# Kernel tuning notes

Measured on AMD Instinct MI355X. Metric: run time of the kernel, lower is better.

## Reference

```python
import jax, jax.numpy as jnp
import numpy as np

N_QUBITS = 4 + 4  # 8
N_LAYERS = 4
DIM = 2 ** N_QUBITS


def _apply_1q(state, U, wire):
    # state: (B, 2,...,2) complex; U: (2,2) complex; contract qubit `wire`
    s = jnp.moveaxis(state, wire + 1, -1)
    s = s @ U.T  # out[..., i] = sum_j U[i, j] * s[..., j]
    return jnp.moveaxis(s, -1, wire + 1)


def _apply_cnot(state, c, t):
    s = jnp.moveaxis(state, (c + 1, t + 1), (-2, -1))  # (..., 2c, 2t)
    s = jnp.concatenate([s[..., 0:1, :], s[..., 1:2, ::-1]], axis=-2)
    return jnp.moveaxis(s, (-2, -1), (c + 1, t + 1))


def _quantum_layer(q_in, qw):
    """Batched statevector sim: RY(pi*x) encoding + StronglyEntanglingLayers + <Z_i>."""
    B = q_in.shape[0]
    # RY(a)|0> = cos(a/2)|0> + sin(a/2)|1>, a = pi * x  -> product state
    half = q_in * (jnp.pi / 2)
    qvecs = jnp.stack([jnp.cos(half), jnp.sin(half)], axis=-1).astype(jnp.complex64)  # (B, n, 2)
    state = qvecs[:, 0]
    for i in range(1, N_QUBITS):
        state = (state[:, :, None] * qvecs[:, i][:, None, :]).reshape(B, -1)
    state = state.reshape((B,) + (2,) * N_QUBITS)
    # Rot(phi, theta, omega) = RZ(omega) RY(theta) RZ(phi)
    phi, theta, omega = qw[..., 0], qw[..., 1], qw[..., 2]
    c, s = jnp.cos(theta / 2), jnp.sin(theta / 2)
    m00 = jnp.exp(-0.5j * (phi + omega)) * c
    m01 = -jnp.exp(0.5j * (phi - omega)) * s
    m10 = jnp.exp(-0.5j * (phi - omega)) * s
    m11 = jnp.exp(0.5j * (phi + omega)) * c
    rot = jnp.stack([jnp.stack([m00, m01], -1), jnp.stack([m10, m11], -1)], -2)  # (L, n, 2, 2)
    rot = rot.astype(jnp.complex64)
    for l in range(N_LAYERS):
        for w in range(N_QUBITS):
            state = _apply_1q(state, rot[l, w], w)
        r = (l % (N_QUBITS - 1)) + 1  # PennyLane default ranges
        for w in range(N_QUBITS):
            state = _apply_cnot(state, w, (w + r) % N_QUBITS)
    amps = state.reshape(B, DIM)
    probs = jnp.real(amps * jnp.conj(amps))  # (B, 2^n) float32
    # <Z_i> = sum_b probs_b * (+1 if bit_i(b)==0 else -1); wire 0 = most significant axis
    idx = np.arange(DIM)
    bits = (idx[None, :] >> (N_QUBITS - 1 - np.arange(N_QUBITS))[:, None]) & 1  # (n, 2^n)
    zvals = jnp.asarray(1.0 - 2.0 * bits, dtype=jnp.float32)
    return probs @ zvals.T  # (B, n)


def _forward(x, w_pre1, b_pre1, w_pre2, b_pre2, w_pre3, b_pre3, qw,
             w_post1, b_post1, w_post2, b_post2, w_post3, b_post3):
    # eval mode: dropout is identity
    h = jax.nn.relu(x @ w_pre1 + b_pre1)
    h = jax.nn.relu(h @ w_pre2 + b_pre2)
    q_in = jnp.tanh(h @ w_pre3 + b_pre3)          # (B, n_qubits)
    z = _quantum_layer(q_in, qw)                   # (B, n_qubits)
    h = jax.nn.relu(z @ w_post1 + b_post1)
    h = jax.nn.relu(h @ w_post2 + b_post2)
    return h @ w_post3 + b_post3                   # (B, num_classes)


def setup_inputs() -> dict:
    key = jax.random.key(0)
    ks = jax.random.split(key, 16)
    B, D_IN, C = 16384, 41, 5
    def lin(k, fan_in, fan_out):
        lim = 1.0 / np.sqrt(fan_in)
        k1, k2 = jax.random.split(k)
        return (jax.random.uniform(k1, (fan_in, fan_out), jnp.float32, -lim, lim),
                jax.random.uniform(k2, (fan_out,), jnp.float32, -lim, lim))
    x = jax.random.normal(ks[0], (B, D_IN), jnp.float32)
    w_pre1, b_pre1 = lin(ks[1], D_IN, 64)
    w_pre2, b_pre2 = lin(ks[2], 64, 32)
    w_pre3, b_pre3 = lin(ks[3], 32, N_QUBITS)
    qw = jax.random.normal(ks[4], (N_LAYERS, N_QUBITS, 3), jnp.float32) * 0.1
    w_post1, b_post1 = lin(ks[5], N_QUBITS, 32)
    w_post2, b_post2 = lin(ks[6], 32, 16)
    w_post3, b_post3 = lin(ks[7], 16, C)
    return dict(x=x, w_pre1=w_pre1, b_pre1=b_pre1, w_pre2=w_pre2, b_pre2=b_pre2,
                w_pre3=w_pre3, b_pre3=b_pre3, qw=qw,
                w_post1=w_post1, b_post1=b_post1, w_post2=w_post2, b_post2=b_post2,
                w_post3=w_post3, b_post3=b_post3)


def reference(x, w_pre1, b_pre1, w_pre2, b_pre2, w_pre3, b_pre3, qw,
              w_post1, b_post1, w_post2, b_post2, w_post3, b_post3):
    return _forward(x, w_pre1, b_pre1, w_pre2, b_pre2, w_pre3, b_pre3, qw,
                    w_post1, b_post1, w_post2, b_post2, w_post3, b_post3)
```

## Files before the change

### kernel.cpp

```cpp
#include <hip/hip_runtime.h>
#include <math.h>

#define PI_HALF 1.57079632679489662f

typedef float v2f __attribute__((ext_vector_type(2)));


__device__ __forceinline__ v2f sp(float x) { v2f r; r.x = x; r.y = x; return r; }
__device__ __forceinline__ v2f pkfma(v2f a, v2f b, v2f c) {
  return __builtin_elementwise_fma(a, b, c);
}

template <int CTRL>
__device__ __forceinline__ float dpp_mov(float v) {
  int r = __builtin_amdgcn_update_dpp(0, __float_as_int(v), CTRL, 0xf, 0xf, true);
  return __int_as_float(r);
}
template <int CTRL, int BANK>
__device__ __forceinline__ float mdpp(float old_, float src) {
  int r = __builtin_amdgcn_update_dpp(__float_as_int(old_), __float_as_int(src),
                                      CTRL, 0xf, BANK, false);
  return __int_as_float(r);
}

template <int MASK>
__device__ __forceinline__ float lane_xor(float v) {
  if constexpr (MASK == 1) return dpp_mov<0xB1>(v);
  else if constexpr (MASK == 2) return dpp_mov<0x4E>(v);
  else if constexpr (MASK == 8) return dpp_mov<0x128>(v);
  else return dpp_mov<0x1B>(dpp_mov<0x141>(v));
}
template <int MASK>
__device__ __forceinline__ v2f dpp2(v2f v) {
  v2f r; r.x = lane_xor<MASK>(v.x); r.y = lane_xor<MASK>(v.y); return r;
}

template <int W>
__device__ __forceinline__ void rot_lane(v2f (&RE)[8], v2f (&IM)[8],
                                         const float4 mA, int g) {
  constexpr int LM = 1 << (3 - W);
  const unsigned bit = (g >> (3 - W)) & 1u;
  const int sgn = (int)(bit << 31);
  v2f Av = sp(mA.x);
  v2f Bv = sp(__int_as_float(__float_as_int(mA.y) ^ sgn));
  v2f Cv = sp(__int_as_float(__float_as_int(mA.z) ^ sgn));
  v2f Dv = sp(mA.w);
#pragma unroll
  for (int j = 0; j < 8; ++j) {
    v2f pr = dpp2<LM>(RE[j]);
    v2f pi = dpp2<LM>(IM[j]);
    v2f nr = pkfma(-Dv, pi, pkfma(Cv, pr, pkfma(-Bv, IM[j], Av * RE[j])));
    v2f ni = pkfma( Dv, pr, pkfma(Cv, pi, pkfma( Bv, RE[j], Av * IM[j])));
    RE[j] = nr; IM[j] = ni;
  }
}

template <int JM>
__device__ __forceinline__ void rot_regj(v2f (&RE)[8], v2f (&IM)[8],
                                         const float4 mA) {
  v2f M0r = sp(mA.x), M0i = sp(mA.y), M1r = sp(mA.z), M1i = sp(mA.w);
#pragma unroll
  for (int j = 0; j < 8; ++j) {
    if (!(j & JM)) {
      const int j1 = j | JM;
      v2f r0 = RE[j], i0 = IM[j], r1 = RE[j1], i1 = IM[j1];
      RE[j]  = pkfma(-M1i, i1, pkfma(M1r, r1, pkfma(-M0i, i0, M0r * r0)));
      IM[j]  = pkfma( M1i, r1, pkfma(M1r, i1, pkfma( M0i, r0, M0r * i0)));
      RE[j1] = pkfma( M0i, i1, pkfma(M0r, r1, pkfma(-M1i, i0, (-M1r) * r0)));
      IM[j1] = pkfma(-M0i, r1, pkfma(M0r, i1, pkfma( M1i, r0, (-M1r) * i0)));
    }
  }
}

__device__ __forceinline__ void rot_regh(v2f (&RE)[8], v2f (&IM)[8],
                                         const float4 mA) {
#pragma unroll
  for (int j = 0; j < 8; ++j) {
    float r0 = RE[j].x, i0 = IM[j].x, r1 = RE[j].y, i1 = IM[j].y;
    RE[j].x = fmaf(-mA.w, i1, fmaf(mA.z, r1, fmaf(-mA.y, i0, mA.x * r0)));
    IM[j].x = fmaf( mA.w, r1, fmaf(mA.z, i1, fmaf( mA.y, r0, mA.x * i0)));
    RE[j].y = fmaf( mA.y, i1, fmaf(mA.x, r1, fmaf(-mA.w, i0, -mA.z * r0)));
    IM[j].y = fmaf(-mA.y, r1, fmaf(mA.x, i1, fmaf( mA.w, r0, -mA.z * i0)));
  }
}

template <int GPOS, int LM>
__device__ __forceinline__ void cnot_LL(v2f (&RE)[8], v2f (&IM)[8], int g) {
  if constexpr (GPOS >= 2) {
    constexpr int BANK = (GPOS == 3) ? 0xC : 0xA;
    if constexpr (LM == 4) {
#pragma unroll
      for (int j = 0; j < 8; ++j) {
        float t0 = dpp_mov<0x141>(RE[j].x);
        float t1 = dpp_mov<0x141>(RE[j].y);
        float t2 = dpp_mov<0x141>(IM[j].x);
        float t3 = dpp_mov<0x141>(IM[j].y);
        RE[j].x = mdpp<0x1B, BANK>(RE[j].x, t0);
        RE[j].y = mdpp<0x1B, BANK>(RE[j].y, t1);
        IM[j].x = mdpp<0x1B, BANK>(IM[j].x, t2);
        IM[j].y = mdpp<0x1B, BANK>(IM[j].y, t3);
      }
    } else {
      constexpr int CTRL = (LM == 1) ? 0xB1 : (LM == 2) ? 0x4E : 0x128;
#pragma unroll
      for (int j = 0; j < 8; ++j) {
        RE[j].x = mdpp<CTRL, BANK>(RE[j].x, RE[j].x);
        RE[j].y = mdpp<CTRL, BANK>(RE[j].y, RE[j].y);
        IM[j].x = mdpp<CTRL, BANK>(IM[j].x, IM[j].x);
        IM[j].y = mdpp<CTRL, BANK>(IM[j].y, IM[j].y);
      }
    }
  } else {
    constexpr int CTRL =
        (GPOS == 1 && LM == 1) ? 0xB4 :
        (GPOS == 1 && LM == 2) ? 0x44 :
        (GPOS == 0 && LM == 1) ? 0xA0 :
                                 0x6C;
#pragma unroll
    for (int j = 0; j < 8; ++j) {
      RE[j].x = dpp_mov<CTRL>(RE[j].x);
      RE[j].y = dpp_mov<CTRL>(RE[j].y);
      IM[j].x = dpp_mov<CTRL>(IM[j].x);
      IM[j].y = dpp_mov<CTRL>(IM[j].y);
    }
  }
}

template <int GPOS, int JM>
__device__ __forceinline__ void cnot_LR(v2f (&RE)[8], v2f (&IM)[8], int g) {
  const bool cb = (g >> GPOS) & 1;
#pragma unroll
  for (int j = 0; j < 8; ++j) {
    if (!(j & JM)) {
      const int j1 = j | JM;
      v2f r0 = RE[j], r1 = RE[j1];
      RE[j] = cb ? r1 : r0;  RE[j1] = cb ? r0 : r1;
      v2f i0 = IM[j], i1 = IM[j1];
      IM[j] = cb ? i1 : i0;  IM[j1] = cb ? i0 : i1;
    }
  }
}
template <int GPOS>
__device__ __forceinline__ void cnot_LH(v2f (&RE)[8], v2f (&IM)[8], int g) {
  const bool cb = (g >> GPOS) & 1;
#pragma unroll
  for (int j = 0; j < 8; ++j) {
    v2f r = RE[j]; v2f rs; rs.x = r.y; rs.y = r.x;
    RE[j] = cb ? rs : r;
    v2f i = IM[j]; v2f is2; is2.x = i.y; is2.y = i.x;
    IM[j] = cb ? is2 : i;
  }
}
template <int JC, int LM>
__device__ __forceinline__ void cnot_RL(v2f (&RE)[8], v2f (&IM)[8]) {
#pragma unroll
  for (int j = 0; j < 8; ++j) {
    if (j & JC) {
      RE[j] = dpp2<LM>(RE[j]);
      IM[j] = dpp2<LM>(IM[j]);
    }
  }
}
template <int JC>
__device__ __forceinline__ void cnot_RH(v2f (&RE)[8], v2f (&IM)[8]) {
#pragma unroll
  for (int j = 0; j < 8; ++j) {
    if (j & JC) {
      v2f r = RE[j]; RE[j].x = r.y; RE[j].y = r.x;
      v2f i = IM[j]; IM[j].x = i.y; IM[j].y = i.x;
    }
  }
}
template <int LM>
__device__ __forceinline__ void cnot_HL(v2f (&RE)[8], v2f (&IM)[8]) {
#pragma unroll
  for (int j = 0; j < 8; ++j) {
    RE[j].y = lane_xor<LM>(RE[j].y);
    IM[j].y = lane_xor<LM>(IM[j].y);
  }
}
template <int JC, int JT>
__device__ __forceinline__ void cnot_RR(v2f (&RE)[8], v2f (&IM)[8]) {
#pragma unroll
  for (int j = 0; j < 8; ++j) {
    if ((j & JC) && !(j & JT)) {
      const int j1 = j | JT;
      v2f t = RE[j]; RE[j] = RE[j1]; RE[j1] = t;
      t = IM[j]; IM[j] = IM[j1]; IM[j1] = t;
    }
  }
}

__device__ __forceinline__ void stage_fence() { __threadfence_block(); }

__global__ __launch_bounds__(256, 2) void hqc_kernel(
    const float* __restrict__ x,
    const float* __restrict__ w1, const float* __restrict__ b1,
    const float* __restrict__ w2, const float* __restrict__ b2,
    const float* __restrict__ w3, const float* __restrict__ b3,
    const float* __restrict__ qw,
    const float* __restrict__ wp1, const float* __restrict__ bp1,
    const float* __restrict__ wp2, const float* __restrict__ bp2,
    const float* __restrict__ wp3, const float* __restrict__ bp3,
    float* __restrict__ out, int B) {
  __shared__ __align__(16) float rotm[32][4];
  __shared__ float xbuf[16][44];
  __shared__ __align__(16) float hbuf[16][68];
  __shared__ float h2buf[16][34];
  __shared__ float qbuf[16][20];
  __shared__ float p1buf[16][34];
  __shared__ float p2buf[16][20];

  const int tid = threadIdx.x;
  const int g = tid & 15;
  const int ls = tid >> 4;
  const int s = blockIdx.x * 16 + ls;
  const bool valid = (s < B);

  if (tid < 32) {
    float phi = qw[tid * 3 + 0];
    float th  = qw[tid * 3 + 1];
    float om  = qw[tid * 3 + 2];
    float st_, ct; sincosf(0.5f * th, &st_, &ct);
    float sa, ca;  sincosf(0.5f * (phi + om), &sa, &ca);
    float sb, cb;  sincosf(0.5f * (phi - om), &sb, &cb);
    rotm[tid][0] =  ca * ct;
    rotm[tid][1] = -sa * ct;
    rotm[tid][2] = -cb * st_;
    rotm[tid][3] = -sb * st_;
  }

  if (valid) {
    xbuf[ls][g]      = x[s * 41 + g];
    xbuf[ls][g + 16] = x[s * 41 + g + 16];
    if (g < 9) xbuf[ls][g + 32] = x[s * 41 + g + 32];
  }
  __syncthreads();

  const float4* w1v = (const float4*)w1;
  float4 bv = ((const float4*)b1)[g];
  v2f aA; aA.x = bv.x; aA.y = bv.y;
  v2f aB; aB.x = bv.z; aB.y = bv.w;
#pragma unroll 8
  for (int k = 0; k < 41; ++k) {
    float xk = xbuf[ls][k];
    float4 wv = w1v[k * 16 + g];
    v2f w01; w01.x = wv.x; w01.y = wv.y;
    v2f w23; w23.x = wv.z; w23.y = wv.w;
    v2f xv = sp(xk);
    aA = pkfma(xv, w01, aA);
    aB = pkfma(xv, w23, aB);
  }
  float4 st4;
  st4.x = fmaxf(aA.x, 0.f); st4.y = fmaxf(aA.y, 0.f);
  st4.z = fmaxf(aB.x, 0.f); st4.w = fmaxf(aB.y, 0.f);
  *(float4*)(&hbuf[ls][4 * g]) = st4;
  stage_fence();

  const v2f* w2v = (const v2f*)w2;
  v2f a2 = ((const v2f*)b2)[g];
#pragma unroll 8
  for (int k = 0; k < 64; ++k)
    a2 = pkfma(sp(hbuf[ls][k]), w2v[k * 16 + g], a2);
  h2buf[ls][2 * g]     = fmaxf(a2.x, 0.f);
  h2buf[ls][2 * g + 1] = fmaxf(a2.y, 0.f);
  stage_fence();

  if (g < 8) {
    float acc = b3[g];
#pragma unroll
    for (int k = 0; k < 32; ++k) acc = fmaf(h2buf[ls][k], w3[k * 8 + g], acc);
    float q = tanhf(acc);
    float sh, ch; sincosf(q * PI_HALF, &sh, &ch);
    qbuf[ls][g]     = ch;
    qbuf[ls][8 + g] = sh;
  }
  stage_fence();

  float cwv[8], swv[8];
#pragma unroll
  for (int w = 0; w < 8; ++w) { cwv[w] = qbuf[ls][w]; swv[w] = qbuf[ls][8 + w]; }
  float lp = 1.0f;
#pragma unroll
  for (int w = 0; w < 4; ++w) lp *= ((g >> (3 - w)) & 1) ? swv[w] : cwv[w];
  float f45[4];
#pragma unroll
  for (int a = 0; a < 4; ++a)
    f45[a] = ((a & 2) ? swv[4] : cwv[4]) * ((a & 1) ? swv[5] : cwv[5]);
  v2f F67[2];
  F67[0].x = cwv[6] * cwv[7]; F67[0].y = cwv[6] * swv[7];
  F67[1].x = swv[6] * cwv[7]; F67[1].y = swv[6] * swv[7];
  v2f RE[8], IM[8];
#pragma unroll
  for (int j = 0; j < 8; ++j) {
    RE[j] = sp(lp * f45[j >> 1]) * F67[j & 1];
    IM[j] = sp(0.0f);
  }

#define RM(L, W) (*(const float4*)(&rotm[(L) * 8 + (W)][0]))
#define ROTS(L)                                                          \
  {                                                                      \
    float4 c0 = RM(L, 0), c1 = RM(L, 1), c2 = RM(L, 2), c3 = RM(L, 3),   \
           c4 = RM(L, 4), c5 = RM(L, 5), c6 = RM(L, 6), c7 = RM(L, 7);   \
    rot_lane<0>(RE, IM, c0, g);                                          \
    rot_lane<1>(RE, IM, c1, g);                                          \
    rot_lane<2>(RE, IM, c2, g);                                          \
    rot_lane<3>(RE, IM, c3, g);                                          \
    rot_regj<4>(RE, IM, c4);                                             \
    rot_regj<2>(RE, IM, c5);                                             \
    rot_regj<1>(RE, IM, c6);                                             \
    rot_regh(RE, IM, c7);                                                \
  }

  ROTS(0)
  cnot_LL<3, 4>(RE, IM, g);  cnot_LL<2, 2>(RE, IM, g);
  cnot_LL<1, 1>(RE, IM, g);  cnot_LR<0, 4>(RE, IM, g);
  cnot_RR<4, 2>(RE, IM);     cnot_RR<2, 1>(RE, IM);
  cnot_RH<1>(RE, IM);        cnot_HL<8>(RE, IM);
  ROTS(1)
  cnot_LL<3, 2>(RE, IM, g);  cnot_LL<2, 1>(RE, IM, g);
  cnot_LR<1, 4>(RE, IM, g);  cnot_LR<0, 2>(RE, IM, g);
  cnot_RR<4, 1>(RE, IM);     cnot_RH<2>(RE, IM);
  cnot_RL<1, 8>(RE, IM);     cnot_HL<4>(RE, IM);
  ROTS(2)
  cnot_LL<3, 1>(RE, IM, g);  cnot_LR<2, 4>(RE, IM, g);
  cnot_LR<1, 2>(RE, IM, g);  cnot_LR<0, 1>(RE, IM, g);
  cnot_RH<4>(RE, IM);        cnot_RL<2, 8>(RE, IM);
  cnot_RL<1, 4>(RE, IM);     cnot_HL<2>(RE, IM);
  ROTS(3)
  cnot_LR<3, 4>(RE, IM, g);  cnot_LR<2, 2>(RE, IM, g);
  cnot_LR<1, 1>(RE, IM, g);  cnot_LH<0>(RE, IM, g);
  cnot_RL<4, 8>(RE, IM);     cnot_RL<2, 4>(RE, IM);
  cnot_RL<1, 2>(RE, IM);     cnot_HL<1>(RE, IM);

  v2f pv[8];
#pragma unroll
  for (int j = 0; j < 8; ++j) pv[j] = pkfma(RE[j], RE[j], IM[j] * IM[j]);
  v2f t01 = pv[0] + pv[1], t23 = pv[2] + pv[3];
  v2f t45 = pv[4] + pv[5], t67 = pv[6] + pv[7];
  v2f tlo = t01 + t23, thi = t45 + t67;
  v2f tv = tlo + thi;
  float tot = tv.x + tv.y;
  float s4 = thi.x + thi.y;
  v2f v5 = t23 + t67; float s5 = v5.x + v5.y;
  v2f v6 = (pv[1] + pv[3]) + (pv[5] + pv[7]);
  float s6 = v6.x + v6.y;
  float s7 = tv.y;
  float zp[8];
  zp[0] = ((g >> 3) & 1) ? -tot : tot;
  zp[1] = ((g >> 2) & 1) ? -tot : tot;
  zp[2] = ((g >> 1) & 1) ? -tot : tot;
  zp[3] = (g & 1) ? -tot : tot;
  zp[4] = fmaf(-2.f, s4, tot);
  zp[5] = fmaf(-2.f, s5, tot);
  zp[6] = fmaf(-2.f, s6, tot);
  zp[7] = fmaf(-2.f, s7, tot);
#pragma unroll
  for (int w = 0; w < 8; ++w) zp[w] += lane_xor<1>(zp[w]);
#pragma unroll
  for (int w = 0; w < 8; ++w) zp[w] += lane_xor<2>(zp[w]);
#pragma unroll
  for (int w = 0; w < 8; ++w) zp[w] += lane_xor<4>(zp[w]);
#pragma unroll
  for (int w = 0; w < 8; ++w) zp[w] += lane_xor<8>(zp[w]);

  const v2f* wp1v = (const v2f*)wp1;
  v2f q1 = ((const v2f*)bp1)[g];
#pragma unroll
  for (int k = 0; k < 8; ++k)
    q1 = pkfma(sp(zp[k]), wp1v[k * 16 + g], q1);
  p1buf[ls][2 * g]     = fmaxf(q1.x, 0.f);
  p1buf[ls][2 * g + 1] = fmaxf(q1.y, 0.f);
  stage_fence();

  float q2 = bp2[g];
#pragma unroll
  for (int k = 0; k < 32; ++k) q2 = fmaf(p1buf[ls][k], wp2[k * 16 + g], q2);
  p2buf[ls][g] = fmaxf(q2, 0.f);
  stage_fence();

  if (g < 5 && valid) {
    float o = bp3[g];
#pragma unroll
    for (int k = 0; k < 16; ++k) o = fmaf(p2buf[ls][k], wp3[k * 5 + g], o);
    out[s * 5 + g] = o;
  }
}

extern "C" void kernel_launch(void* const* d_in, const int* in_sizes, int n_in,
                              void* d_out, int out_size, void* d_ws,
                              size_t ws_size, hipStream_t stream) {
  const float* x   = (const float*)d_in[0];
  const float* w1  = (const float*)d_in[1];
  const float* b1  = (const float*)d_in[2];
  const float* w2  = (const float*)d_in[3];
  const float* b2  = (const float*)d_in[4];
  const float* w3  = (const float*)d_in[5];
  const float* b3  = (const float*)d_in[6];
  const float* qw  = (const float*)d_in[7];
  const float* wp1 = (const float*)d_in[8];
  const float* bp1 = (const float*)d_in[9];
  const float* wp2 = (const float*)d_in[10];
  const float* bp2 = (const float*)d_in[11];
  const float* wp3 = (const float*)d_in[12];
  const float* bp3 = (const float*)d_in[13];
  float* out = (float*)d_out;
  const int B = in_sizes[0] / 41;
  const int blocks = (B + 15) / 16;
  hipLaunchKernelGGL(hqc_kernel, dim3(blocks), dim3(256), 0, stream,
                     x, w1, b1, w2, b2, w3, b3, qw,
                     wp1, bp1, wp2, bp2, wp3, bp3, out, B);
}
```

Before: 42.68 us.

## Precompute circuit unitary and apply it with fp16 MFMA matmul per batch

A separate kernel builds the full 256x256 complex circuit unitary once by simulating the circuit on basis states, storing it in fp16 in the workspace. The main kernel then writes each sample's product-state amplitudes to LDS in fp16 and multiplies them by the unitary with MFMA 16x16x32 instructions, computing Z expectations from the squared magnitudes. This swaps per-sample gate simulation for a dense matmul on matrix cores and doubles samples per block. It adds a second launch and global reads of the 256 KB unitary, and fp16 amplitudes and unitary entries lose precision.

Measured after the change: 63.91 us. 1.5x slower.

```diff
diff --git a/kernel.cpp b/kernel.cpp
--- a/kernel.cpp
+++ b/kernel.cpp
@@ -4,6 +4,8 @@
 #define PI_HALF 1.57079632679489662f
 
 typedef float v2f __attribute__((ext_vector_type(2)));
+typedef _Float16 h8 __attribute__((ext_vector_type(8)));
+typedef float f4 __attribute__((ext_vector_type(4)));
 
 
 __device__ __forceinline__ v2f sp(float x) { v2f r; r.x = x; r.y = x; return r; }
@@ -16,13 +18,12 @@
   int r = __builtin_amdgcn_update_dpp(0, __float_as_int(v), CTRL, 0xf, 0xf, true);
   return __int_as_float(r);
 }
-template <int CTRL, int BANK>
+template <int CTRL, int ROW, int BANK>
 __device__ __forceinline__ float mdpp(float old_, float src) {
   int r = __builtin_amdgcn_update_dpp(__float_as_int(old_), __float_as_int(src),
-                                      CTRL, 0xf, BANK, false);
+                                      CTRL, ROW, BANK, false);
   return __int_as_float(r);
 }
-
 template <int MASK>
 __device__ __forceinline__ float lane_xor(float v) {
   if constexpr (MASK == 1) return dpp_mov<0xB1>(v);
@@ -54,7 +55,6 @@
     RE[j] = nr; IM[j] = ni;
   }
 }
-
 template <int JM>
 __device__ __forceinline__ void rot_regj(v2f (&RE)[8], v2f (&IM)[8],
                                          const float4 mA) {
@@ -71,7 +71,6 @@
     }
   }
 }
-
 __device__ __forceinline__ void rot_regh(v2f (&RE)[8], v2f (&IM)[8],
                                          const float4 mA) {
 #pragma unroll
@@ -83,7 +82,6 @@
     IM[j].y = fmaf(-mA.y, r1, fmaf(mA.x, i1, fmaf( mA.w, r0, -mA.z * i0)));
   }
 }
-
 template <int GPOS, int LM>
 __device__ __forceinline__ void cnot_LL(v2f (&RE)[8], v2f (&IM)[8], int g) {
   if constexpr (GPOS >= 2) {
@@ -95,19 +93,19 @@
         float t1 = dpp_mov<0x141>(RE[j].y);
         float t2 = dpp_mov<0x141>(IM[j].x);
         float t3 = dpp_mov<0x141>(IM[j].y);
-        RE[j].x = mdpp<0x1B, BANK>(RE[j].x, t0);
-        RE[j].y = mdpp<0x1B, BANK>(RE[j].y, t1);
-        IM[j].x = mdpp<0x1B, BANK>(IM[j].x, t2);
-        IM[j].y = mdpp<0x1B, BANK>(IM[j].y, t3);
+        RE[j].x = mdpp<0x1B, 0xF, BANK>(RE[j].x, t0);
+        RE[j].y = mdpp<0x1B, 0xF, BANK>(RE[j].y, t1);
+        IM[j].x = mdpp<0x1B, 0xF, BANK>(IM[j].x, t2);
+        IM[j].y = mdpp<0x1B, 0xF, BANK>(IM[j].y, t3);
       }
     } else {
       constexpr int CTRL = (LM == 1) ? 0xB1 : (LM == 2) ? 0x4E : 0x128;
 #pragma unroll
       for (int j = 0; j < 8; ++j) {
-        RE[j].x = mdpp<CTRL, BANK>(RE[j].x, RE[j].x);
-        RE[j].y = mdpp<CTRL, BANK>(RE[j].y, RE[j].y);
-        IM[j].x = mdpp<CTRL, BANK>(IM[j].x, IM[j].x);
-        IM[j].y = mdpp<CTRL, BANK>(IM[j].y, IM[j].y);
+        RE[j].x = mdpp<CTRL, 0xF, BANK>(RE[j].x, RE[j].x);
+        RE[j].y = mdpp<CTRL, 0xF, BANK>(RE[j].y, RE[j].y);
+        IM[j].x = mdpp<CTRL, 0xF, BANK>(IM[j].x, IM[j].x);
+        IM[j].y = mdpp<CTRL, 0xF, BANK>(IM[j].y, IM[j].y);
       }
     }
   } else {
@@ -125,7 +123,6 @@
     }
   }
 }
-
 template <int GPOS, int JM>
 __device__ __forceinline__ void cnot_LR(v2f (&RE)[8], v2f (&IM)[8], int g) {
   const bool cb = (g >> GPOS) & 1;
@@ -193,29 +190,35 @@
 
 __device__ __forceinline__ void stage_fence() { __threadfence_block(); }
 
-__global__ __launch_bounds__(256, 2) void hqc_kernel(
-    const float* __restrict__ x,
-    const float* __restrict__ w1, const float* __restrict__ b1,
-    const float* __restrict__ w2, const float* __restrict__ b2,
-    const float* __restrict__ w3, const float* __restrict__ b3,
-    const float* __restrict__ qw,
-    const float* __restrict__ wp1, const float* __restrict__ bp1,
-    const float* __restrict__ wp2, const float* __restrict__ bp2,
-    const float* __restrict__ wp3, const float* __restrict__ bp3,
-    float* __restrict__ out, int B) {
+#define CIRCUIT_BODY(RE, IM, g)                                        \
+  ROTS(0)                                                              \
+  cnot_LL<3, 4>(RE, IM, g);  cnot_LL<2, 2>(RE, IM, g);                 \
+  cnot_LL<1, 1>(RE, IM, g);  cnot_LR<0, 4>(RE, IM, g);                 \
+  cnot_RR<4, 2>(RE, IM);     cnot_RR<2, 1>(RE, IM);                    \
+  cnot_RH<1>(RE, IM);        cnot_HL<8>(RE, IM);                       \
+  ROTS(1)                                                              \
+  cnot_LL<3, 2>(RE, IM, g);  cnot_LL<2, 1>(RE, IM, g);                 \
+  cnot_LR<1, 4>(RE, IM, g);  cnot_LR<0, 2>(RE, IM, g);                 \
+  cnot_RR<4, 1>(RE, IM);     cnot_RH<2>(RE, IM);                       \
+  cnot_RL<1, 8>(RE, IM);     cnot_HL<4>(RE, IM);                       \
+  ROTS(2)                                                              \
+  cnot_LL<3, 1>(RE, IM, g);  cnot_LR<2, 4>(RE, IM, g);                 \
+  cnot_LR<1, 2>(RE, IM, g);  cnot_LR<0, 1>(RE, IM, g);                 \
+  cnot_RH<4>(RE, IM);        cnot_RL<2, 8>(RE, IM);                    \
+  cnot_RL<1, 4>(RE, IM);     cnot_HL<2>(RE, IM);                       \
+  ROTS(3)                                                              \
+  cnot_LR<3, 4>(RE, IM, g);  cnot_LR<2, 2>(RE, IM, g);                 \
+  cnot_LR<1, 1>(RE, IM, g);  cnot_LH<0>(RE, IM, g);                    \
+  cnot_RL<4, 8>(RE, IM);     cnot_RL<2, 4>(RE, IM);                    \
+  cnot_RL<1, 2>(RE, IM);     cnot_HL<1>(RE, IM);
+
+__global__ __launch_bounds__(256) void build_u_kernel(
+    const float* __restrict__ qw, _Float16* __restrict__ Bt) {
   __shared__ __align__(16) float rotm[32][4];
-  __shared__ float xbuf[16][44];
-  __shared__ __align__(16) float hbuf[16][68];
-  __shared__ float h2buf[16][34];
-  __shared__ float qbuf[16][20];
-  __shared__ float p1buf[16][34];
-  __shared__ float p2buf[16][20];
-
   const int tid = threadIdx.x;
   const int g = tid & 15;
   const int ls = tid >> 4;
-  const int s = blockIdx.x * 16 + ls;
-  const bool valid = (s < B);
+  const int c = blockIdx.x * 16 + ls;
 
   if (tid < 32) {
     float phi = qw[tid * 3 + 0];
@@ -229,6 +232,68 @@
     rotm[tid][2] = -cb * st_;
     rotm[tid][3] = -sb * st_;
   }
+  __syncthreads();
+
+  v2f RE[8], IM[8];
+#pragma unroll
+  for (int j = 0; j < 8; ++j) {
+    RE[j].x = (c == g * 16 + 2 * j)     ? 1.0f : 0.0f;
+    RE[j].y = (c == g * 16 + 2 * j + 1) ? 1.0f : 0.0f;
+    IM[j] = sp(0.0f);
+  }
+
+#define RM(L, W) (*(const float4*)(&rotm[(L) * 8 + (W)][0]))
+#define ROTS(L)                                                          \
+  {                                                                      \
+    float4 c0 = RM(L, 0), c1 = RM(L, 1), c2 = RM(L, 2), c3 = RM(L, 3),   \
+           c4 = RM(L, 4), c5 = RM(L, 5), c6 = RM(L, 6), c7 = RM(L, 7);   \
+    rot_lane<0>(RE, IM, c0, g);                                          \
+    rot_lane<1>(RE, IM, c1, g);                                          \
+    rot_lane<2>(RE, IM, c2, g);                                          \
+    rot_lane<3>(RE, IM, c3, g);                                          \
+    rot_regj<4>(RE, IM, c4);                                             \
+    rot_regj<2>(RE, IM, c5);                                             \
+    rot_regj<1>(RE, IM, c6);                                             \
+    rot_regh(RE, IM, c7);                                                \
+  }
+  CIRCUIT_BODY(RE, IM, g)
+#undef ROTS
+#undef RM
+
+#pragma unroll
+  for (int j = 0; j < 8; ++j) {
+    const int i0 = g * 16 + 2 * j;
+    Bt[i0 * 256 + c]             = (_Float16)RE[j].x;
+    Bt[(i0 + 1) * 256 + c]       = (_Float16)RE[j].y;
+    Bt[(256 + i0) * 256 + c]     = (_Float16)IM[j].x;
+    Bt[(256 + i0 + 1) * 256 + c] = (_Float16)IM[j].y;
+  }
+}
+
+__global__ __launch_bounds__(512) void hqc_main(
+    const float* __restrict__ x,
+    const float* __restrict__ w1, const float* __restrict__ b1,
+    const float* __restrict__ w2, const float* __restrict__ b2,
+    const float* __restrict__ w3, const float* __restrict__ b3,
+    const _Float16* __restrict__ Bt,
+    const float* __restrict__ wp1, const float* __restrict__ bp1,
+    const float* __restrict__ wp2, const float* __restrict__ bp2,
+    const float* __restrict__ wp3, const float* __restrict__ bp3,
+    float* __restrict__ out, int B) {
+  __shared__ __align__(16) _Float16 A_lds[32][264];
+  __shared__ float xbuf[32][44];
+  __shared__ __align__(16) float hbuf[32][68];
+  __shared__ float h2buf[32][34];
+  __shared__ float qbuf[32][20];
+  __shared__ float z_lds[4][32][8];
+  __shared__ float p1buf[32][34];
+  __shared__ float p2buf[32][20];
+
+  const int tid = threadIdx.x;
+  const int g = tid & 15;
+  const int ls = tid >> 4;
+  const int s = blockIdx.x * 32 + ls;
+  const bool valid = (s < B);
 
   if (valid) {
     xbuf[ls][g]      = x[s * 41 + g];
@@ -277,92 +342,107 @@
   }
   stage_fence();
 
-  float cwv[8], swv[8];
-#pragma unroll
-  for (int w = 0; w < 8; ++w) { cwv[w] = qbuf[ls][w]; swv[w] = qbuf[ls][8 + w]; }
-  float lp = 1.0f;
-#pragma unroll
-  for (int w = 0; w < 4; ++w) lp *= ((g >> (3 - w)) & 1) ? swv[w] : cwv[w];
-  float f45[4];
-#pragma unroll
-  for (int a = 0; a < 4; ++a)
-    f45[a] = ((a & 2) ? swv[4] : cwv[4]) * ((a & 1) ? swv[5] : cwv[5]);
-  v2f F67[2];
-  F67[0].x = cwv[6] * cwv[7]; F67[0].y = cwv[6] * swv[7];
-  F67[1].x = swv[6] * cwv[7]; F67[1].y = swv[6] * swv[7];
-  v2f RE[8], IM[8];
-#pragma unroll
-  for (int j = 0; j < 8; ++j) {
-    RE[j] = sp(lp * f45[j >> 1]) * F67[j & 1];
-    IM[j] = sp(0.0f);
-  }
-
-#define RM(L, W) (*(const float4*)(&rotm[(L) * 8 + (W)][0]))
-#define ROTS(L)                                                          \
-  {                                                                      \
-    float4 c0 = RM(L, 0), c1 = RM(L, 1), c2 = RM(L, 2), c3 = RM(L, 3),   \
-           c4 = RM(L, 4), c5 = RM(L, 5), c6 = RM(L, 6), c7 = RM(L, 7);   \
-    rot_lane<0>(RE, IM, c0, g);                                          \
-    rot_lane<1>(RE, IM, c1, g);                                          \
-    rot_lane<2>(RE, IM, c2, g);                                          \
-    rot_lane<3>(RE, IM, c3, g);                                          \
-    rot_regj<4>(RE, IM, c4);                                             \
-    rot_regj<2>(RE, IM, c5);                                             \
-    rot_regj<1>(RE, IM, c6);                                             \
-    rot_regh(RE, IM, c7);                                                \
-  }
-
-  ROTS(0)
-  cnot_LL<3, 4>(RE, IM, g);  cnot_LL<2, 2>(RE, IM, g);
-  cnot_LL<1, 1>(RE, IM, g);  cnot_LR<0, 4>(RE, IM, g);
-  cnot_RR<4, 2>(RE, IM);     cnot_RR<2, 1>(RE, IM);
-  cnot_RH<1>(RE, IM);        cnot_HL<8>(RE, IM);
-  ROTS(1)
-  cnot_LL<3, 2>(RE, IM, g);  cnot_LL<2, 1>(RE, IM, g);
-  cnot_LR<1, 4>(RE, IM, g);  cnot_LR<0, 2>(RE, IM, g);
-  cnot_RR<4, 1>(RE, IM);     cnot_RH<2>(RE, IM);
-  cnot_RL<1, 8>(RE, IM);     cnot_HL<4>(RE, IM);
-  ROTS(2)
-  cnot_LL<3, 1>(RE, IM, g);  cnot_LR<2, 4>(RE, IM, g);
-  cnot_LR<1, 2>(RE, IM, g);  cnot_LR<0, 1>(RE, IM, g);
-  cnot_RH<4>(RE, IM);        cnot_RL<2, 8>(RE, IM);
-  cnot_RL<1, 4>(RE, IM);     cnot_HL<2>(RE, IM);
-  ROTS(3)
-  cnot_LR<3, 4>(RE, IM, g);  cnot_LR<2, 2>(RE, IM, g);
-  cnot_LR<1, 1>(RE, IM, g);  cnot_LH<0>(RE, IM, g);
-  cnot_RL<4, 8>(RE, IM);     cnot_RL<2, 4>(RE, IM);
-  cnot_RL<1, 2>(RE, IM);     cnot_HL<1>(RE, IM);
-
-  v2f pv[8];
-#pragma unroll
-  for (int j = 0; j < 8; ++j) pv[j] = pkfma(RE[j], RE[j], IM[j] * IM[j]);
-  v2f t01 = pv[0] + pv[1], t23 = pv[2] + pv[3];
-  v2f t45 = pv[4] + pv[5], t67 = pv[6] + pv[7];
-  v2f tlo = t01 + t23, thi = t45 + t67;
-  v2f tv = tlo + thi;
-  float tot = tv.x + tv.y;
-  float s4 = thi.x + thi.y;
-  v2f v5 = t23 + t67; float s5 = v5.x + v5.y;
-  v2f v6 = (pv[1] + pv[3]) + (pv[5] + pv[7]);
-  float s6 = v6.x + v6.y;
-  float s7 = tv.y;
+  {
+    float cwv[8], swv[8];
+#pragma unroll
+    for (int w = 0; w < 8; ++w) { cwv[w] = qbuf[ls][w]; swv[w] = qbuf[ls][8 + w]; }
+    float lp = 1.0f;
+#pragma unroll
+    for (int w = 0; w < 4; ++w) lp *= ((g >> (3 - w)) & 1) ? swv[w] : cwv[w];
+    float f45[4];
+#pragma unroll
+    for (int a = 0; a < 4; ++a)
+      f45[a] = ((a & 2) ? swv[4] : cwv[4]) * ((a & 1) ? swv[5] : cwv[5]);
+    v2f F67[2];
+    F67[0].x = cwv[6] * cwv[7]; F67[0].y = cwv[6] * swv[7];
+    F67[1].x = swv[6] * cwv[7]; F67[1].y = swv[6] * swv[7];
+#pragma unroll
+    for (int j = 0; j < 8; ++j) {
+      v2f amp = sp(lp * f45[j >> 1]) * F67[j & 1];
+      A_lds[ls][g * 16 + 2 * j]     = (_Float16)amp.x;
+      A_lds[ls][g * 16 + 2 * j + 1] = (_Float16)amp.y;
+    }
+  }
+  __syncthreads();
+
+  {
+    const int l = tid & 63;
+    const int w = tid >> 6;
+    const int mt = w & 1;
+    const int pgrp = w >> 1;
+    const int cN = l & 15;
+    const int rgrp = l >> 4;
+    const int kb = rgrp * 8;
+
+    float4 zlo[4], zhi[4];
+#pragma unroll
+    for (int v = 0; v < 4; ++v) {
+      zlo[v] = make_float4(0.f, 0.f, 0.f, 0.f);
+      zhi[v] = make_float4(0.f, 0.f, 0.f, 0.f);
+    }
+    const float4 csgn = make_float4((cN & 8) ? -1.f : 1.f, (cN & 4) ? -1.f : 1.f,
+                                    (cN & 2) ? -1.f : 1.f, (cN & 1) ? -1.f : 1.f);
+    const _Float16* Arow = &A_lds[mt * 16 + cN][0];
+
+#pragma unroll
+    for (int t = 0; t < 4; ++t) {
+      const int p = pgrp + 4 * t;
+      const float4 psgn = make_float4((p & 8) ? -1.f : 1.f, (p & 4) ? -1.f : 1.f,
+                                      (p & 2) ? -1.f : 1.f, (p & 1) ? -1.f : 1.f);
+      f4 accr = {0.f, 0.f, 0.f, 0.f};
+      f4 acci = {0.f, 0.f, 0.f, 0.f};
+      const _Float16* brow = Bt + (p * 16 + cN) * 256;
+      const _Float16* irow = Bt + ((256 + p * 16) + cN) * 256;
+#pragma unroll
+      for (int kt = 0; kt < 8; ++kt) {
+        const int kk = kt * 32 + kb;
+        h8 av = *(const h8*)(Arow + kk);
+        h8 br = *(const h8*)(brow + kk);
+        h8 bi = *(const h8*)(irow + kk);
+        accr = __builtin_amdgcn_mfma_f32_16x16x32_f16(av, br, accr, 0, 0, 0);
+        acci = __builtin_amdgcn_mfma_f32_16x16x32_f16(av, bi, acci, 0, 0, 0);
+      }
+#pragma unroll
+      for (int v = 0; v < 4; ++v) {
+        float tot = fmaf(accr[v], accr[v], acci[v] * acci[v]);
+        zlo[v].x = fmaf(tot, psgn.x, zlo[v].x);
+        zlo[v].y = fmaf(tot, psgn.y, zlo[v].y);
+        zlo[v].z = fmaf(tot, psgn.z, zlo[v].z);
+        zlo[v].w = fmaf(tot, psgn.w, zlo[v].w);
+        zhi[v].x = fmaf(tot, csgn.x, zhi[v].x);
+        zhi[v].y = fmaf(tot, csgn.y, zhi[v].y);
+        zhi[v].z = fmaf(tot, csgn.z, zhi[v].z);
+        zhi[v].w = fmaf(tot, csgn.w, zhi[v].w);
+      }
+    }
+
+#define RED(M)                                                          \
+  _Pragma("unroll")                                                     \
+  for (int v = 0; v < 4; ++v) {                                         \
+    zlo[v].x += lane_xor<M>(zlo[v].x); zlo[v].y += lane_xor<M>(zlo[v].y); \
+    zlo[v].z += lane_xor<M>(zlo[v].z); zlo[v].w += lane_xor<M>(zlo[v].w); \
+    zhi[v].x += lane_xor<M>(zhi[v].x); zhi[v].y += lane_xor<M>(zhi[v].y); \
+    zhi[v].z += lane_xor<M>(zhi[v].z); zhi[v].w += lane_xor<M>(zhi[v].w); \
+  }
+    RED(1) RED(2) RED(4) RED(8)
+#undef RED
+
+    if (cN == 0) {
+#pragma unroll
+      for (int v = 0; v < 4; ++v) {
+        const int smp = mt * 16 + rgrp * 4 + v;
+        *(float4*)&z_lds[pgrp][smp][0] = zlo[v];
+        *(float4*)&z_lds[pgrp][smp][4] = zhi[v];
+      }
+    }
+  }
+  __syncthreads();
+
   float zp[8];
-  zp[0] = ((g >> 3) & 1) ? -tot : tot;
-  zp[1] = ((g >> 2) & 1) ? -tot : tot;
-  zp[2] = ((g >> 1) & 1) ? -tot : tot;
-  zp[3] = (g & 1) ? -tot : tot;
-  zp[4] = fmaf(-2.f, s4, tot);
-  zp[5] = fmaf(-2.f, s5, tot);
-  zp[6] = fmaf(-2.f, s6, tot);
-  zp[7] = fmaf(-2.f, s7, tot);
-#pragma unroll
-  for (int w = 0; w < 8; ++w) zp[w] += lane_xor<1>(zp[w]);
-#pragma unroll
-  for (int w = 0; w < 8; ++w) zp[w] += lane_xor<2>(zp[w]);
-#pragma unroll
-  for (int w = 0; w < 8; ++w) zp[w] += lane_xor<4>(zp[w]);
-#pragma unroll
-  for (int w = 0; w < 8; ++w) zp[w] += lane_xor<8>(zp[w]);
+#pragma unroll
+  for (int k = 0; k < 8; ++k)
+    zp[k] = (z_lds[0][ls][k] + z_lds[1][ls][k]) +
+            (z_lds[2][ls][k] + z_lds[3][ls][k]);
 
   const v2f* wp1v = (const v2f*)wp1;
   v2f q1 = ((const v2f*)bp1)[g];
@@ -405,9 +485,13 @@
   const float* wp3 = (const float*)d_in[12];
   const float* bp3 = (const float*)d_in[13];
   float* out = (float*)d_out;
+  _Float16* Bt = (_Float16*)d_ws;
   const int B = in_sizes[0] / 41;
-  const int blocks = (B + 15) / 16;
-  hipLaunchKernelGGL(hqc_kernel, dim3(blocks), dim3(256), 0, stream,
-                     x, w1, b1, w2, b2, w3, b3, qw,
+
+  hipLaunchKernelGGL(build_u_kernel, dim3(16), dim3(256), 0, stream, qw, Bt);
+
+  const int blocks = (B + 31) / 32;
+  hipLaunchKernelGGL(hqc_main, dim3(blocks), dim3(512), 0, stream,
+                     x, w1, b1, w2, b2, w3, b3, Bt,
                      wp1, bp1, wp2, bp2, wp3, bp3, out, B);
 }
```
